# Kernel optimization log

Measured on AMD Instinct MI355X. Metric: run time of the kernel, lower is better.

## Reference

```python
import jax, jax.numpy as jnp
import numpy as np

V, E, C, L, H, I = 50304, 512, 256, 6, 8, 1024
D = C // H            # head_dim = 32
ROT = int(D * 0.25)   # rotary_ndims = 8
B, S = 4, 1024


def _ln(x, w, b, eps=1e-5):
    m = x.mean(-1, keepdims=True)
    v = ((x - m) ** 2).mean(-1, keepdims=True)
    return (x - m) * jax.lax.rsqrt(v + eps) * w + b


def _apply_rope(x, cos, sin):
    # x: [B,S,H,D]; GPT-NeoX partial rotary on first ROT dims
    xr, xp = x[..., :ROT], x[..., ROT:]
    half = ROT // 2
    xrh = jnp.concatenate([-xr[..., half:], xr[..., :half]], -1)
    return jnp.concatenate([xr * cos + xrh * sin, xp], -1)


def setup_inputs() -> dict:
    key = jax.random.key(0)
    ks = jax.random.split(key, 16)
    std = 0.02
    inp = {
        'input_ids': jax.random.randint(ks[0], (B, S), 0, V),
        'prev_context': jnp.zeros((B, C), jnp.float32),
        'embed_w': jax.random.normal(ks[1], (V, E)) * std,
        'en_w': jnp.ones((E,)), 'en_b': jnp.zeros((E,)),
        # ContextBlock: Linear(context_dim+embed_dim -> context_dim) + GELU + LayerNorm
        'ctx_w': jax.random.normal(ks[2], (C, C + E)) * std,
        'ctx_b': jnp.zeros((C,)),
        'cn_w': jnp.ones((C,)), 'cn_b': jnp.zeros((C,)),
        # stacked per-layer Pythia params [L, ...]
        'ln1_w': jnp.ones((L, C)), 'ln1_b': jnp.zeros((L, C)),
        'ln2_w': jnp.ones((L, C)), 'ln2_b': jnp.zeros((L, C)),
        'qkv_w': jax.random.normal(ks[3], (L, 3 * C, C)) * std,
        'qkv_b': jnp.zeros((L, 3 * C)),
        'ao_w': jax.random.normal(ks[4], (L, C, C)) * std,
        'ao_b': jnp.zeros((L, C)),
        'fc1_w': jax.random.normal(ks[5], (L, I, C)) * std,
        'fc1_b': jnp.zeros((L, I)),
        'fc2_w': jax.random.normal(ks[6], (L, C, I)) * std,
        'fc2_b': jnp.zeros((L, C)),
        'fln_w': jnp.ones((C,)), 'fln_b': jnp.zeros((C,)),
        'out_w': jax.random.normal(ks[7], (V, C)) * std,
    }
    return inp


def reference(input_ids, prev_context, embed_w, en_w, en_b, ctx_w, ctx_b, cn_w, cn_b,
              ln1_w, ln1_b, ln2_w, ln2_b, qkv_w, qkv_b, ao_w, ao_b,
              fc1_w, fc1_b, fc2_w, fc2_b, fln_w, fln_b, out_w):
    b, s = input_ids.shape
    tok = _ln(embed_w[input_ids], en_w, en_b)                 # [B,S,E]

    # sequential context recurrence (scan == the per-token Python loop)
    def step(ctx, emb_t):
        h = jnp.concatenate([ctx, emb_t], -1) @ ctx_w.T + ctx_b
        ctx_new = _ln(jax.nn.gelu(h), cn_w, cn_b)
        return ctx_new, ctx_new
    _, hs = jax.lax.scan(step, prev_context, tok.transpose(1, 0, 2))
    x = hs.transpose(1, 0, 2)                                 # [B,S,C]

    pos = jnp.arange(s)
    inv = 1.0 / (10000.0 ** (jnp.arange(0, ROT, 2, dtype=jnp.float32) / ROT))
    ang = pos[:, None] * inv                                  # [S, ROT/2]
    cos = jnp.tile(jnp.cos(ang), (1, 2))[None, :, None, :]
    sin = jnp.tile(jnp.sin(ang), (1, 2))[None, :, None, :]
    causal = jnp.tril(jnp.ones((s, s), bool))

    for l in range(L):
        # parallel residual Pythia/GPT-NeoX layer
        a_in = _ln(x, ln1_w[l], ln1_b[l])
        qkv = jnp.einsum('bsc,oc->bso', a_in, qkv_w[l]) + qkv_b[l]
        q, k, v = [t.reshape(b, s, H, D) for t in jnp.split(qkv, 3, -1)]
        q = _apply_rope(q, cos, sin)
        k = _apply_rope(k, cos, sin)
        sc = jnp.einsum('bqhd,bkhd->bhqk', q, k) / jnp.sqrt(jnp.float32(D))
        sc = jnp.where(causal, sc, jnp.float32(-1e9))
        p = jax.nn.softmax(sc, -1)
        o = jnp.einsum('bhqk,bkhd->bqhd', p, v).reshape(b, s, C)
        attn = o @ ao_w[l].T + ao_b[l]
        m_in = _ln(x, ln2_w[l], ln2_b[l])
        mlp = jax.nn.gelu(m_in @ fc1_w[l].T + fc1_b[l]) @ fc2_w[l].T + fc2_b[l]
        x = x + attn + mlp

    x = _ln(x, fln_w, fln_b)
    logits = jnp.einsum('bsc,vc->bsv', x, out_w)              # [B,S,V]
    return logits
```

## Files before the change

### kernel.cpp

```cpp
#include <hip/hip_runtime.h>

typedef __bf16 bf16x8 __attribute__((ext_vector_type(8)));
typedef float  f32x4  __attribute__((ext_vector_type(4)));
typedef unsigned uint32x4 __attribute__((ext_vector_type(4)));

#define DEV __device__ __forceinline__

DEV ushort f2bf(float f) {
  unsigned u = __builtin_bit_cast(unsigned, f);
  u += 0x7FFFu + ((u >> 16) & 1u);
  return (ushort)(u >> 16);
}
DEV float bf2f(ushort u) { return __builtin_bit_cast(float, ((unsigned)u) << 16); }
DEV unsigned pk2(ushort a, ushort b) { return (unsigned)a | ((unsigned)b << 16); }

DEV f32x4 mfma16(bf16x8 a, bf16x8 b, f32x4 c) {
  return __builtin_amdgcn_mfma_f32_16x16x32_bf16(a, b, c, 0, 0, 0);
}

DEV float gelu_f(float x) {
  float u = 0.7978845608028654f * (x + 0.044715f * x * x * x);
  return x / (1.f + __expf(-2.f * u));
}

#define SEQ  1024
#define NBAT 4
#define CDIM 256
#define EDIM 512
#define NLAY 6
#define NHEAD 8
#define HDIM 32
#define IDIM 1024
#define NVOC 50304
#define NROWS (NBAT * SEQ)

__global__ __launch_bounds__(256) void cvt_k(const float* __restrict__ src,
                                             ushort* __restrict__ dst, int n4) {
  int i = blockIdx.x * blockDim.x + threadIdx.x;
  int stride = gridDim.x * blockDim.x;
  for (; i < n4; i += stride) {
    float4 f = ((const float4*)src)[i];
    ushort4 u; u.x = f2bf(f.x); u.y = f2bf(f.y); u.z = f2bf(f.z); u.w = f2bf(f.w);
    ((ushort4*)dst)[i] = u;
  }
}

__global__ __launch_bounds__(64) void embed_ln_k(const int* __restrict__ ids,
                                                 const float* __restrict__ ew,
                                                 const float* __restrict__ w,
                                                 const float* __restrict__ b,
                                                 ushort* __restrict__ tok) {
  int m = blockIdx.x, t = threadIdx.x;
  const float* row = ew + (size_t)ids[m] * EDIM;
  float4 v0 = *(const float4*)(row + t * 8);
  float4 v1 = *(const float4*)(row + t * 8 + 4);
  float sm = v0.x + v0.y + v0.z + v0.w + v1.x + v1.y + v1.z + v1.w;
  float sq = v0.x*v0.x + v0.y*v0.y + v0.z*v0.z + v0.w*v0.w
           + v1.x*v1.x + v1.y*v1.y + v1.z*v1.z + v1.w*v1.w;
#pragma unroll
  for (int msk = 1; msk <= 32; msk <<= 1) { sm += __shfl_xor(sm, msk); sq += __shfl_xor(sq, msk); }
  float mean = sm * (1.f / EDIM);
  float var  = sq * (1.f / EDIM) - mean * mean;
  float inv  = rsqrtf(var + 1e-5f);
  float4 w0 = *(const float4*)(w + t * 8), w1 = *(const float4*)(w + t * 8 + 4);
  float4 b0 = *(const float4*)(b + t * 8), b1 = *(const float4*)(b + t * 8 + 4);
  ushort4 u0, u1;
  u0.x = f2bf((v0.x - mean) * inv * w0.x + b0.x);
  u0.y = f2bf((v0.y - mean) * inv * w0.y + b0.y);
  u0.z = f2bf((v0.z - mean) * inv * w0.z + b0.z);
  u0.w = f2bf((v0.w - mean) * inv * w0.w + b0.w);
  u1.x = f2bf((v1.x - mean) * inv * w1.x + b1.x);
  u1.y = f2bf((v1.y - mean) * inv * w1.y + b1.y);
  u1.z = f2bf((v1.z - mean) * inv * w1.z + b1.z);
  u1.w = f2bf((v1.w - mean) * inv * w1.w + b1.w);
  *(ushort4*)(tok + (size_t)m * EDIM + t * 8)     = u0;
  *(ushort4*)(tok + (size_t)m * EDIM + t * 8 + 4) = u1;
}

template <bool DUAL>
__global__ __launch_bounds__(256) void ln_k(const float* __restrict__ x,
                                            const float* __restrict__ w1, const float* __restrict__ b1,
                                            const float* __restrict__ w2, const float* __restrict__ b2,
                                            ushort* __restrict__ o1, ushort* __restrict__ o2) {
  int wave = threadIdx.x >> 6, t = threadIdx.x & 63;
  int m = blockIdx.x * 4 + wave;
  const float* row = x + (size_t)m * CDIM;
  float4 v = *(const float4*)(row + t * 4);
  float sm = v.x + v.y + v.z + v.w;
  float sq = v.x*v.x + v.y*v.y + v.z*v.z + v.w*v.w;
#pragma unroll
  for (int msk = 1; msk <= 32; msk <<= 1) { sm += __shfl_xor(sm, msk); sq += __shfl_xor(sq, msk); }
  float mean = sm * (1.f / CDIM);
  float var  = sq * (1.f / CDIM) - mean * mean;
  float inv  = rsqrtf(var + 1e-5f);
  float n0 = (v.x - mean) * inv, n1 = (v.y - mean) * inv, n2 = (v.z - mean) * inv, n3 = (v.w - mean) * inv;
  {
    float4 wv = *(const float4*)(w1 + t * 4), bv = *(const float4*)(b1 + t * 4);
    ushort4 u; u.x = f2bf(n0*wv.x+bv.x); u.y = f2bf(n1*wv.y+bv.y); u.z = f2bf(n2*wv.z+bv.z); u.w = f2bf(n3*wv.w+bv.w);
    *(ushort4*)(o1 + (size_t)m * CDIM + t * 4) = u;
  }
  if constexpr (DUAL) {
    float4 wv = *(const float4*)(w2 + t * 4), bv = *(const float4*)(b2 + t * 4);
    ushort4 u; u.x = f2bf(n0*wv.x+bv.x); u.y = f2bf(n1*wv.y+bv.y); u.z = f2bf(n2*wv.z+bv.z); u.w = f2bf(n3*wv.w+bv.w);
    *(ushort4*)(o2 + (size_t)m * CDIM + t * 4) = u;
  }
}

enum { GF_BIAS = 1, GF_GELU = 2, GF_ACC = 4, GF_BF16O = 8, GF_WF32 = 16 };

template <int FLAGS>
__global__ __launch_bounds__(256) void gemm_k(const ushort* __restrict__ A, int lda,
                                              const void* __restrict__ Wv, int ldw,
                                              const float* __restrict__ bias,
                                              void* __restrict__ C, int ldc, int K) {
  __shared__ __attribute__((aligned(16))) ushort lsA[128 * 32];
  __shared__ __attribute__((aligned(16))) ushort lsB[128 * 32];
  const int tid = threadIdx.x, lane = tid & 63, wave = tid >> 6;
  const int wm = wave >> 1, wn = wave & 1;
  const int row0 = blockIdx.x * 128, col0 = blockIdx.y * 128;
  const int l15 = lane & 15, koff = (lane >> 4) * 8;

  f32x4 acc[4][4] = {};
  for (int k0 = 0; k0 < K; k0 += 32) {
    __syncthreads();
#pragma unroll
    for (int p = 0; p < 2; ++p) {
      int c = tid + p * 256;
      int r = c >> 2, k8 = (c & 3) * 8;
      *(uint4*)(&lsA[c * 8]) = *(const uint4*)(A + (size_t)(row0 + r) * lda + k0 + k8);
      if constexpr (FLAGS & GF_WF32) {
        const float* gw = (const float*)Wv + (size_t)(col0 + r) * ldw + k0 + k8;
        float4 f0 = *(const float4*)gw, f1 = *(const float4*)(gw + 4);
        uint4 vw;
        vw.x = pk2(f2bf(f0.x), f2bf(f0.y)); vw.y = pk2(f2bf(f0.z), f2bf(f0.w));
        vw.z = pk2(f2bf(f1.x), f2bf(f1.y)); vw.w = pk2(f2bf(f1.z), f2bf(f1.w));
        *(uint4*)(&lsB[c * 8]) = vw;
      } else {
        *(uint4*)(&lsB[c * 8]) = *(const uint4*)((const ushort*)Wv + (size_t)(col0 + r) * ldw + k0 + k8);
      }
    }
    __syncthreads();
    bf16x8 af[4], bfr[4];
#pragma unroll
    for (int mt = 0; mt < 4; ++mt)
      af[mt] = __builtin_bit_cast(bf16x8, *(const uint4*)(&lsA[(wm * 64 + mt * 16 + l15) * 32 + koff]));
#pragma unroll
    for (int nt = 0; nt < 4; ++nt)
      bfr[nt] = __builtin_bit_cast(bf16x8, *(const uint4*)(&lsB[(wn * 64 + nt * 16 + l15) * 32 + koff]));
#pragma unroll
    for (int mt = 0; mt < 4; ++mt)
#pragma unroll
      for (int nt = 0; nt < 4; ++nt)
        acc[mt][nt] = mfma16(af[mt], bfr[nt], acc[mt][nt]);
  }
#pragma unroll
  for (int mt = 0; mt < 4; ++mt) {
#pragma unroll
    for (int nt = 0; nt < 4; ++nt) {
      int col = col0 + wn * 64 + nt * 16 + l15;
      float bv = (FLAGS & GF_BIAS) ? bias[col] : 0.f;
      int rowb = row0 + wm * 64 + mt * 16 + (lane >> 4) * 4;
#pragma unroll
      for (int r = 0; r < 4; ++r) {
        float v = acc[mt][nt][r] + bv;
        if constexpr (FLAGS & GF_GELU) v = gelu_f(v);
        size_t off = (size_t)(rowb + r) * ldc + col;
        if constexpr (FLAGS & GF_ACC)        ((float*)C)[off] += v;
        else if constexpr (FLAGS & GF_BF16O) ((ushort*)C)[off] = f2bf(v);
        else                                 ((float*)C)[off] = v;
      }
    }
  }
}

template <int FLAGS>
__global__ __launch_bounds__(256) void gemm64_k(const ushort* __restrict__ A, int lda,
                                                const void* __restrict__ Wv, int ldw,
                                                const float* __restrict__ bias,
                                                void* __restrict__ C, int ldc, int K) {
  __shared__ __attribute__((aligned(16))) ushort lsA[64 * 32];
  __shared__ __attribute__((aligned(16))) ushort lsB[64 * 32];
  const int tid = threadIdx.x, lane = tid & 63, wave = tid >> 6;
  const int row0 = blockIdx.x * 64, col0 = blockIdx.y * 64;
  const int l15 = lane & 15, lhi = lane >> 4, koff = lhi * 8;

  f32x4 acc[4] = {};
  for (int k0 = 0; k0 < K; k0 += 32) {
    __syncthreads();
    {
      int r = tid >> 2, k8 = (tid & 3) * 8;
      *(uint4*)(&lsA[tid * 8]) = *(const uint4*)(A + (size_t)(row0 + r) * lda + k0 + k8);
      if constexpr (FLAGS & GF_WF32) {
        const float* gw = (const float*)Wv + (size_t)(col0 + r) * ldw + k0 + k8;
        float4 f0 = *(const float4*)gw, f1 = *(const float4*)(gw + 4);
        uint4 vw;
        vw.x = pk2(f2bf(f0.x), f2bf(f0.y)); vw.y = pk2(f2bf(f0.z), f2bf(f0.w));
        vw.z = pk2(f2bf(f1.x), f2bf(f1.y)); vw.w = pk2(f2bf(f1.z), f2bf(f1.w));
        *(uint4*)(&lsB[tid * 8]) = vw;
      } else {
        *(uint4*)(&lsB[tid * 8]) = *(const uint4*)((const ushort*)Wv + (size_t)(col0 + r) * ldw + k0 + k8);
      }
    }
    __syncthreads();
    bf16x8 af = __builtin_bit_cast(bf16x8, *(const uint4*)(&lsA[(wave * 16 + l15) * 32 + koff]));
#pragma unroll
    for (int nt = 0; nt < 4; ++nt) {
      bf16x8 bfr = __builtin_bit_cast(bf16x8, *(const uint4*)(&lsB[(nt * 16 + l15) * 32 + koff]));
      acc[nt] = mfma16(af, bfr, acc[nt]);
    }
  }
#pragma unroll
  for (int nt = 0; nt < 4; ++nt) {
    int col = col0 + nt * 16 + l15;
    float bv = (FLAGS & GF_BIAS) ? bias[col] : 0.f;
    int rowb = row0 + wave * 16 + lhi * 4;
#pragma unroll
    for (int r = 0; r < 4; ++r) {
      float v = acc[nt][r] + bv;
      if constexpr (FLAGS & GF_GELU) v = gelu_f(v);
      size_t off = (size_t)(rowb + r) * ldc + col;
      if constexpr (FLAGS & GF_ACC)        ((float*)C)[off] += v;
      else if constexpr (FLAGS & GF_BF16O) ((ushort*)C)[off] = f2bf(v);
      else                                 ((float*)C)[off] = v;
    }
  }
}

__global__ __launch_bounds__(256) void qkvrope_k(const ushort* __restrict__ A,
                                                 const float* __restrict__ W,
                                                 const float* __restrict__ bias,
                                                 ushort* __restrict__ Qo,
                                                 ushort* __restrict__ Ko,
                                                 ushort* __restrict__ Vt) {
  __shared__ __attribute__((aligned(16))) ushort lsA[64 * 32];
  __shared__ __attribute__((aligned(16))) ushort lsB[64 * 32];
  const int tid = threadIdx.x, lane = tid & 63, wave = tid >> 6;
  const int row0 = blockIdx.x * 64, col0 = blockIdx.y * 64;
  const int l15 = lane & 15, lhi = lane >> 4, koff = lhi * 8;

  f32x4 acc[4] = {};
  for (int k0 = 0; k0 < CDIM; k0 += 32) {
    __syncthreads();
    {
      int r = tid >> 2, k8 = (tid & 3) * 8;
      *(uint4*)(&lsA[tid * 8]) = *(const uint4*)(A + (size_t)(row0 + r) * CDIM + k0 + k8);
      const float* gw = W + (size_t)(col0 + r) * CDIM + k0 + k8;
      float4 f0 = *(const float4*)gw, f1 = *(const float4*)(gw + 4);
      uint4 vw;
      vw.x = pk2(f2bf(f0.x), f2bf(f0.y)); vw.y = pk2(f2bf(f0.z), f2bf(f0.w));
      vw.z = pk2(f2bf(f1.x), f2bf(f1.y)); vw.w = pk2(f2bf(f1.z), f2bf(f1.w));
      *(uint4*)(&lsB[tid * 8]) = vw;
    }
    __syncthreads();
    bf16x8 af = __builtin_bit_cast(bf16x8, *(const uint4*)(&lsA[(wave * 16 + l15) * 32 + koff]));
#pragma unroll
    for (int nt = 0; nt < 4; ++nt) {
      bf16x8 bfr = __builtin_bit_cast(bf16x8, *(const uint4*)(&lsB[(nt * 16 + l15) * 32 + koff]));
      acc[nt] = mfma16(af, bfr, acc[nt]);
    }
  }
  const int rowb = row0 + wave * 16 + lhi * 4;
  const int b = rowb >> 10, s0 = rowb & 1023;
#pragma unroll
  for (int nt = 0; nt < 4; ++nt) {
    int c = col0 + nt * 16 + l15;
    int which = c >> 8;
    int h = (c >> 5) & 7;
    int d = c & 31;
    size_t bh = (size_t)(b * NHEAD + h);
    float bv = bias[c];
    float val[4], part[4];
#pragma unroll
    for (int r = 0; r < 4; ++r) val[r] = acc[nt][r] + bv;
#pragma unroll
    for (int r = 0; r < 4; ++r) part[r] = __shfl_xor(val[r], 4);
    if (d < 8 && which < 2) {
      float sgn = (d < 4) ? -1.f : 1.f;
      int j = d & 3;
      float invp = (j == 0) ? 1.f : (j == 1) ? 0.1f : (j == 2) ? 0.01f : 0.001f;
#pragma unroll
      for (int r = 0; r < 4; ++r) {
        float ang = (float)(s0 + r) * invp;
        float cs, sn;
        __sincosf(ang, &sn, &cs);
        val[r] = val[r] * cs + sgn * part[r] * sn;
      }
    }
    if (which == 2) {
      ushort4 u; u.x = f2bf(val[0]); u.y = f2bf(val[1]); u.z = f2bf(val[2]); u.w = f2bf(val[3]);
      *(ushort4*)(Vt + bh * HDIM * SEQ + (size_t)d * SEQ + s0) = u;
    } else {
      ushort* dst = (which == 0) ? Qo : Ko;
#pragma unroll
      for (int r = 0; r < 4; ++r)
        dst[(bh * SEQ + s0 + r) * HDIM + d] = f2bf(val[r]);
    }
  }
}

__global__ __launch_bounds__(256) void gemm64_dual_k(const ushort* __restrict__ A1, int lda1,
                                                     const float* __restrict__ W1, int ldw1, int K1,
                                                     const ushort* __restrict__ A2, int lda2,
                                                     const float* __restrict__ W2, int ldw2, int K2,
                                                     const float* __restrict__ b1,
                                                     const float* __restrict__ b2,
                                                     float* __restrict__ C, int ldc) {
  __shared__ __attribute__((aligned(16))) ushort lsA[64 * 32];
  __shared__ __attribute__((aligned(16))) ushort lsB[64 * 32];
  const int tid = threadIdx.x, lane = tid & 63, wave = tid >> 6;
  const int row0 = blockIdx.x * 64, col0 = blockIdx.y * 64;
  const int l15 = lane & 15, lhi = lane >> 4, koff = lhi * 8;

  f32x4 acc[4] = {};
  for (int k0 = 0; k0 < K1 + K2; k0 += 32) {
    __syncthreads();
    {
      int r = tid >> 2, k8 = (tid & 3) * 8;
      const ushort* Ap; const float* Wp; int kk;
      if (k0 < K1) { Ap = A1 + (size_t)(row0 + r) * lda1; Wp = W1 + (size_t)(col0 + r) * ldw1; kk = k0 + k8; }
      else         { Ap = A2 + (size_t)(row0 + r) * lda2; Wp = W2 + (size_t)(col0 + r) * ldw2; kk = k0 - K1 + k8; }
      *(uint4*)(&lsA[tid * 8]) = *(const uint4*)(Ap + kk);
      float4 f0 = *(const float4*)(Wp + kk), f1 = *(const float4*)(Wp + kk + 4);
      uint4 vw;
      vw.x = pk2(f2bf(f0.x), f2bf(f0.y)); vw.y = pk2(f2bf(f0.z), f2bf(f0.w));
      vw.z = pk2(f2bf(f1.x), f2bf(f1.y)); vw.w = pk2(f2bf(f1.z), f2bf(f1.w));
      *(uint4*)(&lsB[tid * 8]) = vw;
    }
    __syncthreads();
    bf16x8 af = __builtin_bit_cast(bf16x8, *(const uint4*)(&lsA[(wave * 16 + l15) * 32 + koff]));
#pragma unroll
    for (int nt = 0; nt < 4; ++nt) {
      bf16x8 bfr = __builtin_bit_cast(bf16x8, *(const uint4*)(&lsB[(nt * 16 + l15) * 32 + koff]));
      acc[nt] = mfma16(af, bfr, acc[nt]);
    }
  }
#pragma unroll
  for (int nt = 0; nt < 4; ++nt) {
    int col = col0 + nt * 16 + l15;
    float bv = b1[col] + b2[col];
    int rowb = row0 + wave * 16 + lhi * 4;
#pragma unroll
    for (int r = 0; r < 4; ++r)
      C[(size_t)(rowb + r) * ldc + col] += acc[nt][r] + bv;
  }
}

__global__ __launch_bounds__(256, 1) void scan_k(const float* __restrict__ ctx_w,
                                                 const float* __restrict__ prev_ctx,
                                                 const float* __restrict__ P,
                                                 const float* __restrict__ cn_w,
                                                 const float* __restrict__ cn_b,
                                                 float* __restrict__ x) {
  __shared__ __attribute__((aligned(16))) ushort g_lds[2][4 * 288];
  __shared__ __attribute__((aligned(16))) float  part_lds[2][4][4][2];
  const int tid = threadIdx.x, lane = tid & 63, wave = tid >> 6;
  const int l15 = lane & 15, lhi = lane >> 4;
  const int bb = l15 & 3;
  const int ss = l15 >> 2;
  const int ccol = wave * 64 + ss * 16 + lhi * 4;

  float4 wv  = *(const float4*)(cn_w + ccol);
  float4 bvv = *(const float4*)(cn_b + ccol);
  float s1v[4] = {}, c1v[4] = {};
#pragma unroll 1
  for (int kk = 0; kk < CDIM; kk += 4) {
    float4 wk = *(const float4*)(cn_w + kk);
    float4 bk = *(const float4*)(cn_b + kk);
#pragma unroll
    for (int j = 0; j < 4; ++j) {
      float4 Wr = *(const float4*)(ctx_w + (size_t)(ccol + j) * 768 + kk);
      s1v[j] += Wr.x * wk.x + Wr.y * wk.y + Wr.z * wk.z + Wr.w * wk.w;
      c1v[j] += Wr.x * bk.x + Wr.y * bk.y + Wr.z * bk.z + Wr.w * bk.w;
    }
  }

  {
    float4 c4 = *(const float4*)(prev_ctx + bb * CDIM + ccol);
    ushort4 u; u.x = f2bf(c4.x); u.y = f2bf(c4.y); u.z = f2bf(c4.z); u.w = f2bf(c4.w);
    *(ushort4*)&g_lds[0][bb * 288 + ccol] = u;
  }

  uint32x4 wfu[4][8];
#pragma unroll
  for (int mt = 0; mt < 4; ++mt)
#pragma unroll
    for (int kt = 0; kt < 8; ++kt) {
      const float* s = ctx_w + (size_t)(wave * 64 + mt * 16 + l15) * 768 + kt * 32 + lhi * 8;
      float4 f0 = *(const float4*)s, f1 = *(const float4*)(s + 4);
      uint32x4 vw;
      vw.x = pk2(f2bf(f0.x), f2bf(f0.y)); vw.y = pk2(f2bf(f0.z), f2bf(f0.w));
      vw.z = pk2(f2bf(f1.x), f2bf(f1.y)); vw.w = pk2(f2bf(f1.z), f2bf(f1.w));
      wfu[mt][kt] = vw;
    }
  float4 pf = *(const float4*)(P + ((size_t)bb * SEQ + 0) * CDIM + ccol);
  __syncthreads();

  float gr[4];
  {
    uint32x4 bfr[8];
#pragma unroll
    for (int kt = 0; kt < 8; ++kt)
      bfr[kt] = *(const uint32x4*)(&g_lds[0][bb * 288 + kt * 32 + lhi * 8]);
    f32x4 acc[4] = {};
#pragma unroll
    for (int mt = 0; mt < 4; ++mt)
#pragma unroll
      for (int kt = 0; kt < 8; ++kt)
        acc[mt] = mfma16(__builtin_bit_cast(bf16x8, wfu[mt][kt]),
                         __builtin_bit_cast(bf16x8, bfr[kt]), acc[mt]);
    f32x4 av = (ss == 0) ? acc[0] : (ss == 1) ? acc[1] : (ss == 2) ? acc[2] : acc[3];
    gr[0] = gelu_f(av[0] + pf.x); gr[1] = gelu_f(av[1] + pf.y);
    gr[2] = gelu_f(av[2] + pf.z); gr[3] = gelu_f(av[3] + pf.w);
  }

#pragma unroll
  for (int mt = 0; mt < 4; ++mt)
#pragma unroll
    for (int kt = 0; kt < 8; ++kt) {
      int k = kt * 32 + lhi * 8;
      const float* s = ctx_w + (size_t)(wave * 64 + mt * 16 + l15) * 768 + k;
      float4 f0 = *(const float4*)s, f1 = *(const float4*)(s + 4);
      float4 w0 = *(const float4*)(cn_w + k), w1 = *(const float4*)(cn_w + k + 4);
      uint32x4 vw;
      vw.x = pk2(f2bf(f0.x * w0.x), f2bf(f0.y * w0.y));
      vw.y = pk2(f2bf(f0.z * w0.z), f2bf(f0.w * w0.w));
      vw.z = pk2(f2bf(f1.x * w1.x), f2bf(f1.y * w1.y));
      vw.w = pk2(f2bf(f1.z * w1.z), f2bf(f1.w * w1.w));
      wfu[mt][kt] = vw;
    }
#pragma unroll
  for (int mt = 0; mt < 4; ++mt)
#pragma unroll
    for (int kt = 0; kt < 8; ++kt)
      asm volatile("" : "+v"(wfu[mt][kt]));

  float4 ps0, ps1, ps2, ps3;
  ps1 = *(const float4*)(P + ((size_t)bb * SEQ + 1) * CDIM + ccol);
  ps2 = *(const float4*)(P + ((size_t)bb * SEQ + 2) * CDIM + ccol);
  ps3 = *(const float4*)(P + ((size_t)bb * SEQ + 3) * CDIM + ccol);
  ps0 = ps3;
  __syncthreads();

  {
    ushort4 u; u.x = f2bf(gr[0]); u.y = f2bf(gr[1]); u.z = f2bf(gr[2]); u.w = f2bf(gr[3]);
    *(ushort4*)&g_lds[0][bb * 288 + ccol] = u;
    float lsm = gr[0] + gr[1] + gr[2] + gr[3];
    float lsq = gr[0]*gr[0] + gr[1]*gr[1] + gr[2]*gr[2] + gr[3]*gr[3];
    lsm += __shfl_xor(lsm, 4);  lsq += __shfl_xor(lsq, 4);
    lsm += __shfl_xor(lsm, 8);  lsq += __shfl_xor(lsq, 8);
    lsm += __shfl_xor(lsm, 16); lsq += __shfl_xor(lsq, 16);
    lsm += __shfl_xor(lsm, 32); lsq += __shfl_xor(lsq, 32);
    if (ss == 0 && lhi == 0) {
      part_lds[0][bb][wave][0] = lsm;
      part_lds[0][bb][wave][1] = lsq;
    }
  }
  __syncthreads();

#define SCAN_STEP(T, CUR, NXT, PUSE, PLOAD)                                          \
  {                                                                                  \
    int tp = ((T) + 4 < SEQ) ? (T) + 4 : SEQ - 1;                                    \
    PLOAD = *(const float4*)(P + ((size_t)bb * SEQ + tp) * CDIM + ccol);             \
    uint32x4 bfr[8];                                                                 \
    _Pragma("unroll")                                                                \
    for (int kt = 0; kt < 8; ++kt)                                                   \
      bfr[kt] = *(const uint32x4*)(&g_lds[CUR][bb * 288 + kt * 32 + lhi * 8]);       \
    const float4* pp = (const float4*)&part_lds[CUR][bb][0][0];                      \
    float4 qpa = pp[0], qpb = pp[1];                                                 \
    f32x4 accA[4] = {}, accB[4] = {};                                                \
    _Pragma("unroll")                                                                \
    for (int mt = 0; mt < 4; ++mt) {                                                 \
      accA[mt] = mfma16(__builtin_bit_cast(bf16x8, wfu[mt][0]), __builtin_bit_cast(bf16x8, bfr[0]), accA[mt]); \
      accB[mt] = mfma16(__builtin_bit_cast(bf16x8, wfu[mt][4]), __builtin_bit_cast(bf16x8, bfr[4]), accB[mt]); \
      accA[mt] = mfma16(__builtin_bit_cast(bf16x8, wfu[mt][1]), __builtin_bit_cast(bf16x8, bfr[1]), accA[mt]); \
      accB[mt] = mfma16(__builtin_bit_cast(bf16x8, wfu[mt][5]), __builtin_bit_cast(bf16x8, bfr[5]), accB[mt]); \
      accA[mt] = mfma16(__builtin_bit_cast(bf16x8, wfu[mt][2]), __builtin_bit_cast(bf16x8, bfr[2]), accA[mt]); \
      accB[mt] = mfma16(__builtin_bit_cast(bf16x8, wfu[mt][6]), __builtin_bit_cast(bf16x8, bfr[6]), accB[mt]); \
      accA[mt] = mfma16(__builtin_bit_cast(bf16x8, wfu[mt][3]), __builtin_bit_cast(bf16x8, bfr[3]), accA[mt]); \
      accB[mt] = mfma16(__builtin_bit_cast(bf16x8, wfu[mt][7]), __builtin_bit_cast(bf16x8, bfr[7]), accB[mt]); \
    }                                                                                \
    float sm = (qpa.x + qpa.z) + (qpb.x + qpb.z);                                    \
    float sq = (qpa.y + qpa.w) + (qpb.y + qpb.w);                                    \
    float mu  = sm * (1.f / CDIM);                                                   \
    float inv = rsqrtf(sq * (1.f / CDIM) - mu * mu + 1e-5f);                         \
    float invmu = inv * mu;                                                          \
    float4 y;                                                                        \
    y.x = wv.x * (inv * gr[0] - invmu) + bvv.x;                                      \
    y.y = wv.y * (inv * gr[1] - invmu) + bvv.y;                                      \
    y.z = wv.z * (inv * gr[2] - invmu) + bvv.z;                                      \
    y.w = wv.w * (inv * gr[3] - invmu) + bvv.w;                                      \
    *(float4*)(x + ((size_t)bb * SEQ + (T)) * CDIM + ccol) = y;                      \
    f32x4 avA = (ss == 0) ? accA[0] : (ss == 1) ? accA[1] : (ss == 2) ? accA[2] : accA[3]; \
    f32x4 avB = (ss == 0) ? accB[0] : (ss == 1) ? accB[1] : (ss == 2) ? accB[2] : accB[3]; \
    f32x4 av = avA + avB;                                                            \
    gr[0] = gelu_f(inv * av[0] - invmu * s1v[0] + c1v[0] + PUSE.x);                  \
    gr[1] = gelu_f(inv * av[1] - invmu * s1v[1] + c1v[1] + PUSE.y);                  \
    gr[2] = gelu_f(inv * av[2] - invmu * s1v[2] + c1v[2] + PUSE.z);                  \
    gr[3] = gelu_f(inv * av[3] - invmu * s1v[3] + c1v[3] + PUSE.w);                  \
    {                                                                                \
      ushort4 u; u.x = f2bf(gr[0]); u.y = f2bf(gr[1]); u.z = f2bf(gr[2]); u.w = f2bf(gr[3]); \
      *(ushort4*)&g_lds[NXT][bb * 288 + ccol] = u;                                   \
    }                                                                                \
    float lsm = gr[0] + gr[1] + gr[2] + gr[3];                                       \
    float lsq = gr[0]*gr[0] + gr[1]*gr[1] + gr[2]*gr[2] + gr[3]*gr[3];               \
    lsm += __shfl_xor(lsm, 4);  lsq += __shfl_xor(lsq, 4);                           \
    lsm += __shfl_xor(lsm, 8);  lsq += __shfl_xor(lsq, 8);                           \
    lsm += __shfl_xor(lsm, 16); lsq += __shfl_xor(lsq, 16);                          \
    lsm += __shfl_xor(lsm, 32); lsq += __shfl_xor(lsq, 32);                          \
    if (ss == 0 && lhi == 0) {                                                       \
      part_lds[NXT][bb][wave][0] = lsm;                                              \
      part_lds[NXT][bb][wave][1] = lsq;                                              \
    }                                                                                \
    asm volatile("s_waitcnt lgkmcnt(0)" ::: "memory");                               \
    __builtin_amdgcn_s_barrier();                                                    \
    __builtin_amdgcn_sched_barrier(0);                                               \
  }

  for (int t = 0; t < SEQ; t += 4) {
    SCAN_STEP(t,     0, 1, ps1, ps0)
    SCAN_STEP(t + 1, 1, 0, ps2, ps1)
    SCAN_STEP(t + 2, 0, 1, ps3, ps2)
    SCAN_STEP(t + 3, 1, 0, ps0, ps3)
  }
#undef SCAN_STEP
}

__global__ __launch_bounds__(256) void attn_k(const ushort* __restrict__ Q,
                                              const ushort* __restrict__ K,
                                              const ushort* __restrict__ VT,
                                              ushort* __restrict__ O) {
  __shared__ __attribute__((aligned(16))) ushort Plds[4 * 16 * 64];
  const int tid = threadIdx.x, lane = tid & 63, wave = tid >> 6;
  const int bh = blockIdx.y;
  const int qtile = blockIdx.x + 16 * wave;
  const int q0 = qtile * 16;
  const int l15 = lane & 15, lhi = lane >> 4;
  const float scale = 0.17677669529663689f;

  bf16x8 qa = __builtin_bit_cast(bf16x8,
      *(const uint4*)(Q + ((size_t)bh * SEQ + q0 + l15) * HDIM + lhi * 8));
  const ushort* Kb = K + (size_t)bh * SEQ * HDIM;
  const ushort* Vb = VT + (size_t)bh * HDIM * SEQ;
  ushort* Pw = &Plds[wave * 1024];

  f32x4 o0 = {}, o1 = {};
  float lacc[4] = {};

  for (int kt = 0; kt <= qtile; kt += 4) {
    f32x4 s[4];
    f32x4 z = {};
#pragma unroll
    for (int j = 0; j < 4; ++j) {
      bf16x8 kf = __builtin_bit_cast(bf16x8,
          *(const uint4*)(Kb + (size_t)((kt + j) * 16 + l15) * HDIM + lhi * 8));
      s[j] = mfma16(qa, kf, z);
    }
    float p[4][4];
#pragma unroll
    for (int j = 0; j < 4; ++j) {
      const bool tv = (kt + j <= qtile);
#pragma unroll
      for (int r = 0; r < 4; ++r) {
        int qr = q0 + lhi * 4 + r;
        int kc = (kt + j) * 16 + l15;
        p[j][r] = (tv && kc <= qr) ? __expf(s[j][r] * scale) : 0.f;
        lacc[r] += p[j][r];
      }
    }
#pragma unroll
    for (int j = 0; j < 4; ++j)
#pragma unroll
      for (int r = 0; r < 4; ++r)
        Pw[(lhi * 4 + r) * 64 + j * 16 + l15] = f2bf(p[j][r]);
#pragma unroll
    for (int w = 0; w < 2; ++w) {
      bf16x8 pa  = __builtin_bit_cast(bf16x8, *(const uint4*)(&Pw[l15 * 64 + w * 32 + lhi * 8]));
      bf16x8 v0f = __builtin_bit_cast(bf16x8,
          *(const uint4*)(Vb + (size_t)l15 * SEQ + kt * 16 + w * 32 + lhi * 8));
      bf16x8 v1f = __builtin_bit_cast(bf16x8,
          *(const uint4*)(Vb + (size_t)(16 + l15) * SEQ + kt * 16 + w * 32 + lhi * 8));
      o0 = mfma16(pa, v0f, o0);
      o1 = mfma16(pa, v1f, o1);
    }
  }
#pragma unroll
  for (int msk = 1; msk <= 8; msk <<= 1)
#pragma unroll
    for (int r = 0; r < 4; ++r) lacc[r] += __shfl_xor(lacc[r], msk);

  const int b = bh >> 3, h = bh & 7;
#pragma unroll
  for (int r = 0; r < 4; ++r) {
    float inv = 1.f / lacc[r];
    int qr = q0 + lhi * 4 + r;
    size_t base = ((size_t)(b * SEQ + qr)) * CDIM + h * HDIM;
    O[base + l15]      = f2bf(o0[r] * inv);
    O[base + 16 + l15] = f2bf(o1[r] * inv);
  }
}

static size_t ws_take(size_t& o, size_t bytes) {
  size_t r = o;
  o += (bytes + 255) & ~(size_t)255;
  return r;
}

extern "C" void kernel_launch(void* const* d_in, const int* in_sizes, int n_in,
                              void* d_out, int out_size, void* d_ws, size_t ws_size,
                              hipStream_t stream) {
  (void)in_sizes; (void)n_in; (void)out_size; (void)ws_size;
  const int*   input_ids = (const int*)  d_in[0];
  const float* prev_ctx  = (const float*)d_in[1];
  const float* embed_w   = (const float*)d_in[2];
  const float* en_w      = (const float*)d_in[3];
  const float* en_b      = (const float*)d_in[4];
  const float* ctx_w     = (const float*)d_in[5];
  const float* ctx_b     = (const float*)d_in[6];
  const float* cn_w      = (const float*)d_in[7];
  const float* cn_b      = (const float*)d_in[8];
  const float* ln1_w     = (const float*)d_in[9];
  const float* ln1_b     = (const float*)d_in[10];
  const float* ln2_w     = (const float*)d_in[11];
  const float* ln2_b     = (const float*)d_in[12];
  const float* qkv_w     = (const float*)d_in[13];
  const float* qkv_b     = (const float*)d_in[14];
  const float* ao_w      = (const float*)d_in[15];
  const float* ao_b      = (const float*)d_in[16];
  const float* fc1_w     = (const float*)d_in[17];
  const float* fc1_b     = (const float*)d_in[18];
  const float* fc2_w     = (const float*)d_in[19];
  const float* fc2_b     = (const float*)d_in[20];
  const float* fln_w     = (const float*)d_in[21];
  const float* fln_b     = (const float*)d_in[22];
  const float* out_w     = (const float*)d_in[23];
  float* logits = (float*)d_out;

  char* ws = (char*)d_ws;
  size_t o = 0;
  ushort* WB_OUT = (ushort*)(ws + ws_take(o, (size_t)NVOC * CDIM * 2));
  ushort* TOK    = (ushort*)(ws + ws_take(o, (size_t)NROWS * EDIM * 2));
  float*  PBUF   = (float*) (ws + ws_take(o, (size_t)NROWS * CDIM * 4));
  float*  XBUF   = (float*) (ws + ws_take(o, (size_t)NROWS * CDIM * 4));
  ushort* AIN    = (ushort*)(ws + ws_take(o, (size_t)NROWS * CDIM * 2));
  ushort* MIN    = (ushort*)(ws + ws_take(o, (size_t)NROWS * CDIM * 2));
  ushort* QB     = (ushort*)(ws + ws_take(o, (size_t)NROWS * CDIM * 2));
  ushort* KB     = (ushort*)(ws + ws_take(o, (size_t)NROWS * CDIM * 2));
  ushort* VTB    = (ushort*)(ws + ws_take(o, (size_t)NROWS * CDIM * 2));
  ushort* OB     = (ushort*)(ws + ws_take(o, (size_t)NROWS * CDIM * 2));
  ushort* TBUF   = (ushort*)(ws + ws_take(o, (size_t)NROWS * IDIM * 2));
  ushort* XLN    = (ushort*)(ws + ws_take(o, (size_t)NROWS * CDIM * 2));

  cvt_k<<<dim3(2048), dim3(256), 0, stream>>>(out_w, WB_OUT, NVOC * CDIM / 4);
  embed_ln_k<<<dim3(NROWS), dim3(64), 0, stream>>>(input_ids, embed_w, en_w, en_b, TOK);
  gemm64_k<GF_BIAS | GF_WF32><<<dim3(64, 4), dim3(256), 0, stream>>>(
      TOK, EDIM, (const void*)(ctx_w + 256), 768, ctx_b, (void*)PBUF, CDIM, EDIM);
  scan_k<<<dim3(1), dim3(256), 0, stream>>>(ctx_w, prev_ctx, PBUF, cn_w, cn_b, XBUF);

  for (int l = 0; l < NLAY; ++l) {
    ln_k<true><<<dim3(NROWS / 4), dim3(256), 0, stream>>>(
        XBUF, ln1_w + l * CDIM, ln1_b + l * CDIM, ln2_w + l * CDIM, ln2_b + l * CDIM, AIN, MIN);
    qkvrope_k<<<dim3(64, 12), dim3(256), 0, stream>>>(
        AIN, qkv_w + (size_t)l * 768 * CDIM, qkv_b + l * 768, QB, KB, VTB);
    attn_k<<<dim3(16, 32), dim3(256), 0, stream>>>(QB, KB, VTB, OB);
    gemm64_k<GF_BIAS | GF_GELU | GF_BF16O | GF_WF32><<<dim3(64, 16), dim3(256), 0, stream>>>(
        MIN, CDIM, (const void*)(fc1_w + (size_t)l * IDIM * CDIM), CDIM,
        fc1_b + l * IDIM, (void*)TBUF, IDIM, CDIM);
    gemm64_dual_k<<<dim3(64, 4), dim3(256), 0, stream>>>(
        OB, CDIM, ao_w + (size_t)l * CDIM * CDIM, CDIM, CDIM,
        TBUF, IDIM, fc2_w + (size_t)l * CDIM * IDIM, IDIM, IDIM,
        ao_b + l * CDIM, fc2_b + l * CDIM, XBUF, CDIM);
  }

  ln_k<false><<<dim3(NROWS / 4), dim3(256), 0, stream>>>(
      XBUF, fln_w, fln_b, nullptr, nullptr, XLN, nullptr);
  gemm_k<0><<<dim3(32, 393), dim3(256), 0, stream>>>(
      XLN, CDIM, (const void*)WB_OUT, CDIM, nullptr, (void*)logits, NVOC, CDIM);
}
```

Measured before the change: 1.808 ms.

## Pre-convert all layer weights to bf16 inside the scan kernel's idle blocks

The serial context scan runs on a single block, so it is launched with 256 extra blocks that convert the qkv, attention-out, fc1, fc2 and output-projection weights to bf16 while the scan runs. The per-layer GEMMs then load bf16 weights straight into LDS instead of loading fp32 and converting them on every tile, which halves weight traffic and removes conversion ALU work in the inner loops. The standalone output-weight conversion kernel is removed. The cost is extra workspace, and the conversion blocks may compete with the latency-bound scan block for memory bandwidth.

```diff
diff --git a/kernel.cpp b/kernel.cpp
--- a/kernel.cpp
+++ b/kernel.cpp
@@ -33,17 +33,6 @@
 #define IDIM 1024
 #define NVOC 50304
 #define NROWS (NBAT * SEQ)
-
-__global__ __launch_bounds__(256) void cvt_k(const float* __restrict__ src,
-                                             ushort* __restrict__ dst, int n4) {
-  int i = blockIdx.x * blockDim.x + threadIdx.x;
-  int stride = gridDim.x * blockDim.x;
-  for (; i < n4; i += stride) {
-    float4 f = ((const float4*)src)[i];
-    ushort4 u; u.x = f2bf(f.x); u.y = f2bf(f.y); u.z = f2bf(f.z); u.w = f2bf(f.w);
-    ((ushort4*)dst)[i] = u;
-  }
-}
 
 __global__ __launch_bounds__(64) void embed_ln_k(const int* __restrict__ ids,
                                                  const float* __restrict__ ew,
@@ -227,7 +216,7 @@
 }
 
 __global__ __launch_bounds__(256) void qkvrope_k(const ushort* __restrict__ A,
-                                                 const float* __restrict__ W,
+                                                 const ushort* __restrict__ W,
                                                  const float* __restrict__ bias,
                                                  ushort* __restrict__ Qo,
                                                  ushort* __restrict__ Ko,
@@ -244,12 +233,7 @@
     {
       int r = tid >> 2, k8 = (tid & 3) * 8;
       *(uint4*)(&lsA[tid * 8]) = *(const uint4*)(A + (size_t)(row0 + r) * CDIM + k0 + k8);
-      const float* gw = W + (size_t)(col0 + r) * CDIM + k0 + k8;
-      float4 f0 = *(const float4*)gw, f1 = *(const float4*)(gw + 4);
-      uint4 vw;
-      vw.x = pk2(f2bf(f0.x), f2bf(f0.y)); vw.y = pk2(f2bf(f0.z), f2bf(f0.w));
-      vw.z = pk2(f2bf(f1.x), f2bf(f1.y)); vw.w = pk2(f2bf(f1.z), f2bf(f1.w));
-      *(uint4*)(&lsB[tid * 8]) = vw;
+      *(uint4*)(&lsB[tid * 8]) = *(const uint4*)(W + (size_t)(col0 + r) * CDIM + k0 + k8);
     }
     __syncthreads();
     bf16x8 af = __builtin_bit_cast(bf16x8, *(const uint4*)(&lsA[(wave * 16 + l15) * 32 + koff]));
@@ -299,9 +283,9 @@
 }
 
 __global__ __launch_bounds__(256) void gemm64_dual_k(const ushort* __restrict__ A1, int lda1,
-                                                     const float* __restrict__ W1, int ldw1, int K1,
+                                                     const ushort* __restrict__ W1, int ldw1, int K1,
                                                      const ushort* __restrict__ A2, int lda2,
-                                                     const float* __restrict__ W2, int ldw2, int K2,
+                                                     const ushort* __restrict__ W2, int ldw2, int K2,
                                                      const float* __restrict__ b1,
                                                      const float* __restrict__ b2,
                                                      float* __restrict__ C, int ldc) {
@@ -316,15 +300,11 @@
     __syncthreads();
     {
       int r = tid >> 2, k8 = (tid & 3) * 8;
-      const ushort* Ap; const float* Wp; int kk;
+      const ushort* Ap; const ushort* Wp; int kk;
       if (k0 < K1) { Ap = A1 + (size_t)(row0 + r) * lda1; Wp = W1 + (size_t)(col0 + r) * ldw1; kk = k0 + k8; }
       else         { Ap = A2 + (size_t)(row0 + r) * lda2; Wp = W2 + (size_t)(col0 + r) * ldw2; kk = k0 - K1 + k8; }
       *(uint4*)(&lsA[tid * 8]) = *(const uint4*)(Ap + kk);
-      float4 f0 = *(const float4*)(Wp + kk), f1 = *(const float4*)(Wp + kk + 4);
-      uint4 vw;
-      vw.x = pk2(f2bf(f0.x), f2bf(f0.y)); vw.y = pk2(f2bf(f0.z), f2bf(f0.w));
-      vw.z = pk2(f2bf(f1.x), f2bf(f1.y)); vw.w = pk2(f2bf(f1.z), f2bf(f1.w));
-      *(uint4*)(&lsB[tid * 8]) = vw;
+      *(uint4*)(&lsB[tid * 8]) = *(const uint4*)(Wp + kk);
     }
     __syncthreads();
     bf16x8 af = __builtin_bit_cast(bf16x8, *(const uint4*)(&lsA[(wave * 16 + l15) * 32 + koff]));
@@ -345,12 +325,42 @@
   }
 }
 
-__global__ __launch_bounds__(256, 1) void scan_k(const float* __restrict__ ctx_w,
-                                                 const float* __restrict__ prev_ctx,
-                                                 const float* __restrict__ P,
-                                                 const float* __restrict__ cn_w,
-                                                 const float* __restrict__ cn_b,
-                                                 float* __restrict__ x) {
+DEV void cvt_range(const float* __restrict__ src, ushort* __restrict__ dst,
+                   int n4, int idx, int stride) {
+  for (int i = idx; i < n4; i += stride) {
+    float4 f = ((const float4*)src)[i];
+    ushort4 u; u.x = f2bf(f.x); u.y = f2bf(f.y); u.z = f2bf(f.z); u.w = f2bf(f.w);
+    ((ushort4*)dst)[i] = u;
+  }
+}
+
+__global__ __launch_bounds__(256, 1) void scan_fused_k(const float* __restrict__ ctx_w,
+                                                       const float* __restrict__ prev_ctx,
+                                                       const float* __restrict__ P,
+                                                       const float* __restrict__ cn_w,
+                                                       const float* __restrict__ cn_b,
+                                                       float* __restrict__ x,
+                                                       const float* __restrict__ qkv_w,
+                                                       const float* __restrict__ ao_w,
+                                                       const float* __restrict__ fc1_w,
+                                                       const float* __restrict__ fc2_w,
+                                                       const float* __restrict__ out_w,
+                                                       ushort* __restrict__ WQKV,
+                                                       ushort* __restrict__ WAO,
+                                                       ushort* __restrict__ WFC1,
+                                                       ushort* __restrict__ WFC2,
+                                                       ushort* __restrict__ WOUT) {
+  if (blockIdx.x > 0) {
+    const int idx = (blockIdx.x - 1) * 256 + threadIdx.x;
+    const int stride = (gridDim.x - 1) * 256;
+    cvt_range(qkv_w, WQKV, NLAY * 768 * CDIM / 4, idx, stride);
+    cvt_range(ao_w,  WAO,  NLAY * CDIM * CDIM / 4, idx, stride);
+    cvt_range(fc1_w, WFC1, NLAY * IDIM * CDIM / 4, idx, stride);
+    cvt_range(fc2_w, WFC2, NLAY * CDIM * IDIM / 4, idx, stride);
+    cvt_range(out_w, WOUT, NVOC * CDIM / 4, idx, stride);
+    return;
+  }
+
   __shared__ __attribute__((aligned(16))) ushort g_lds[2][4 * 288];
   __shared__ __attribute__((aligned(16))) float  part_lds[2][4][4][2];
   const int tid = threadIdx.x, lane = tid & 63, wave = tid >> 6;
@@ -638,6 +648,10 @@
   char* ws = (char*)d_ws;
   size_t o = 0;
   ushort* WB_OUT = (ushort*)(ws + ws_take(o, (size_t)NVOC * CDIM * 2));
+  ushort* WQKV   = (ushort*)(ws + ws_take(o, (size_t)NLAY * 768 * CDIM * 2));
+  ushort* WAO    = (ushort*)(ws + ws_take(o, (size_t)NLAY * CDIM * CDIM * 2));
+  ushort* WFC1   = (ushort*)(ws + ws_take(o, (size_t)NLAY * IDIM * CDIM * 2));
+  ushort* WFC2   = (ushort*)(ws + ws_take(o, (size_t)NLAY * CDIM * IDIM * 2));
   ushort* TOK    = (ushort*)(ws + ws_take(o, (size_t)NROWS * EDIM * 2));
   float*  PBUF   = (float*) (ws + ws_take(o, (size_t)NROWS * CDIM * 4));
   float*  XBUF   = (float*) (ws + ws_take(o, (size_t)NROWS * CDIM * 4));
@@ -650,24 +664,25 @@
   ushort* TBUF   = (ushort*)(ws + ws_take(o, (size_t)NROWS * IDIM * 2));
   ushort* XLN    = (ushort*)(ws + ws_take(o, (size_t)NROWS * CDIM * 2));
 
-  cvt_k<<<dim3(2048), dim3(256), 0, stream>>>(out_w, WB_OUT, NVOC * CDIM / 4);
   embed_ln_k<<<dim3(NROWS), dim3(64), 0, stream>>>(input_ids, embed_w, en_w, en_b, TOK);
   gemm64_k<GF_BIAS | GF_WF32><<<dim3(64, 4), dim3(256), 0, stream>>>(
       TOK, EDIM, (const void*)(ctx_w + 256), 768, ctx_b, (void*)PBUF, CDIM, EDIM);
-  scan_k<<<dim3(1), dim3(256), 0, stream>>>(ctx_w, prev_ctx, PBUF, cn_w, cn_b, XBUF);
+  scan_fused_k<<<dim3(257), dim3(256), 0, stream>>>(
+      ctx_w, prev_ctx, PBUF, cn_w, cn_b, XBUF,
+      qkv_w, ao_w, fc1_w, fc2_w, out_w, WQKV, WAO, WFC1, WFC2, WB_OUT);
 
   for (int l = 0; l < NLAY; ++l) {
     ln_k<true><<<dim3(NROWS / 4), dim3(256), 0, stream>>>(
         XBUF, ln1_w + l * CDIM, ln1_b + l * CDIM, ln2_w + l * CDIM, ln2_b + l * CDIM, AIN, MIN);
     qkvrope_k<<<dim3(64, 12), dim3(256), 0, stream>>>(
-        AIN, qkv_w + (size_t)l * 768 * CDIM, qkv_b + l * 768, QB, KB, VTB);
+        AIN, WQKV + (size_t)l * 768 * CDIM, qkv_b + l * 768, QB, KB, VTB);
     attn_k<<<dim3(16, 32), dim3(256), 0, stream>>>(QB, KB, VTB, OB);
-    gemm64_k<GF_BIAS | GF_GELU | GF_BF16O | GF_WF32><<<dim3(64, 16), dim3(256), 0, stream>>>(
-        MIN, CDIM, (const void*)(fc1_w + (size_t)l * IDIM * CDIM), CDIM,
+    gemm64_k<GF_BIAS | GF_GELU | GF_BF16O><<<dim3(64, 16), dim3(256), 0, stream>>>(
+        MIN, CDIM, (const void*)(WFC1 + (size_t)l * IDIM * CDIM), CDIM,
         fc1_b + l * IDIM, (void*)TBUF, IDIM, CDIM);
     gemm64_dual_k<<<dim3(64, 4), dim3(256), 0, stream>>>(
-        OB, CDIM, ao_w + (size_t)l * CDIM * CDIM, CDIM, CDIM,
-        TBUF, IDIM, fc2_w + (size_t)l * CDIM * IDIM, IDIM, IDIM,
+        OB, CDIM, WAO + (size_t)l * CDIM * CDIM, CDIM, CDIM,
+        TBUF, IDIM, WFC2 + (size_t)l * CDIM * IDIM, IDIM, IDIM,
         ao_b + l * CDIM, fc2_b + l * CDIM, XBUF, CDIM);
   }
 
```

Result: faster. 1.684 ms (median of 2 runs) (-6.9%).
